# Kernel tuning notes

Hardware: AMD Instinct MI355X
Metric: run time of the kernel (lower is better)

The kernel has to match this reference:

```python
import jax, jax.numpy as jnp
import numpy as np

WS = 7  # window size of the inner WindowAttention
EPS = 1e-5


def pc_roll(xb, shifts, axis):
    """Per-channel circular roll of [B,C,H,W] along `axis` (2 or 3).
    torch.roll semantics: out[i] = in[(i - shift) % n]."""
    n = xb.shape[axis]
    idx = (jnp.arange(n)[None, :] - shifts[:, None]) % n  # [C, n]
    if axis == 2:
        idxb = jnp.broadcast_to(idx[None, :, :, None], xb.shape)
    else:
        idxb = jnp.broadcast_to(idx[None, :, None, :], xb.shape)
    return jnp.take_along_axis(xb, idxb, axis=axis)


def layernorm(x, w, b):
    m = x.mean(-1, keepdims=True)
    v = x.var(-1, keepdims=True)
    return (x - m) * jax.lax.rsqrt(v + EPS) * w + b


def batchnorm2d(x, g, b):
    # training-mode BN: batch statistics over (B,H,W) per channel
    m = x.mean(axis=(0, 2, 3), keepdims=True)
    v = x.var(axis=(0, 2, 3), keepdims=True)
    return (x - m) * jax.lax.rsqrt(v + EPS) * g[None, :, None, None] + b[None, :, None, None]


def conv1x1(x, w, b):
    # x: [B,C,H,W], w: [Cout,Cin]
    return jnp.einsum('bchw,oc->bohw', x, w) + b[None, :, None, None]


def window_attention(q, k, v):
    # single-head Swin-style window attention, 7x7 windows, no rel-pos bias
    B, C, H, W = q.shape
    nh, nw = H // WS, W // WS

    def part(t):  # [B,C,H,W] -> [B*nh*nw, WS*WS, C]
        t = t.reshape(B, C, nh, WS, nw, WS)
        return t.transpose(0, 2, 4, 3, 5, 1).reshape(B * nh * nw, WS * WS, C)

    qw, kw, vw = part(q), part(k), part(v)
    scale = C ** -0.5
    attn = jax.nn.softmax(jnp.einsum('wnc,wmc->wnm', qw, kw) * scale, axis=-1)
    out = jnp.einsum('wnm,wmc->wnc', attn, vw)
    out = out.reshape(B, nh, nw, WS, WS, C).transpose(0, 5, 1, 3, 2, 4).reshape(B, C, H, W)
    return out


def setup_inputs() -> dict:
    B, H, W, C = 32, 56, 56, 128
    N = H * W
    key = jax.random.key(0)
    ks = jax.random.split(key, 16)
    f32 = jnp.float32

    def lin_w(k, din, dout):
        return 0.02 * jax.random.normal(k, (din, dout), dtype=f32)

    conv_std = float(np.sqrt(2.0 / C))
    inp = {
        'x': jax.random.normal(ks[0], (B, N, C), dtype=f32),
        'fc1_w': lin_w(ks[1], C, C), 'fc1_b': jnp.zeros((C,), f32),
        'fc2_w': lin_w(ks[2], C, C), 'fc2_b': jnp.zeros((C,), f32),
        'fc3_w': lin_w(ks[3], C, C), 'fc3_b': jnp.zeros((C,), f32),
        'fc4_w': lin_w(ks[4], C, C), 'fc4_b': jnp.zeros((C,), f32),
        'fc5_w': lin_w(ks[5], 2 * C, C), 'fc5_b': jnp.zeros((C,), f32),
        'fc6_w': lin_w(ks[6], 2 * C, C), 'fc6_b': jnp.zeros((C,), f32),
        'ln_w': jnp.ones((2 * C,), f32), 'ln_b': jnp.zeros((2 * C,), f32),
        'q_w': conv_std * jax.random.normal(ks[7], (C, C), dtype=f32), 'q_b': jnp.zeros((C,), f32),
        'k_w': conv_std * jax.random.normal(ks[8], (C, C), dtype=f32), 'k_b': jnp.zeros((C,), f32),
        'v_w': conv_std * jax.random.normal(ks[9], (C, C), dtype=f32), 'v_b': jnp.zeros((C,), f32),
        'bn1_g': jnp.ones((C,), f32), 'bn1_b': jnp.zeros((C,), f32),
        'bn2_g': jnp.ones((C,), f32), 'bn2_b': jnp.zeros((C,), f32),
        'H': H, 'W': W,
    }
    return inp


def reference(x, fc1_w, fc1_b, fc2_w, fc2_b, fc3_w, fc3_b, fc4_w, fc4_b,
              fc5_w, fc5_b, fc6_w, fc6_b, ln_w, ln_b,
              q_w, q_b, k_w, k_b, v_w, v_b, bn1_g, bn1_b, bn2_g, bn2_b, H, W):
    B, N, C = x.shape
    shifts = jnp.arange(C)
    gelu = lambda t: jax.nn.gelu(t, approximate=False)

    def to_bchw(t):
        return t.transpose(0, 2, 1).reshape(B, C, H, W)

    def to_bnc(t):
        return t.reshape(B, C, N).transpose(0, 2, 1)

    # branch 1: roll +c along H -> fc1 -> GELU -> roll +c along W -> fc2
    h = to_bnc(pc_roll(to_bchw(x), shifts, axis=2))
    h = gelu(h @ fc1_w + fc1_b)
    h = to_bnc(pc_roll(to_bchw(h), shifts, axis=3))
    x_1 = h @ fc2_w + fc2_b

    # branch 2: roll -c along W -> fc3 -> GELU -> roll +c along H -> fc4
    h = to_bnc(pc_roll(to_bchw(x), -shifts, axis=3))
    h = gelu(h @ fc3_w + fc3_b)
    h = to_bnc(pc_roll(to_bchw(h), shifts, axis=2))
    x_2 = h @ fc4_w + fc4_b

    x_1 = x_1 + x
    x_2 = x_2 + x
    x1 = jnp.concatenate([x_1, x_2], axis=2)          # [B,N,2C]
    x1 = layernorm(x1, ln_w, ln_b)
    x1 = x1 @ fc5_w + fc5_b
    x1 = x1 + x

    # local-attention branch (DWConv module actually runs WindowAtten + BN + ReLU)
    xb = to_bchw(x)
    att = window_attention(conv1x1(xb, q_w, q_b), conv1x1(xb, k_w, k_b), conv1x1(xb, v_w, v_b))
    x2 = jax.nn.relu(batchnorm2d(att, bn1_g, bn1_b))  # DWConv forward
    x2 = jax.nn.relu(x2)                              # act2 (idempotent, kept for fidelity)
    x2 = batchnorm2d(x2, bn2_g, bn2_b)                # norm2
    x2 = x2.reshape(B, C, N).transpose(0, 2, 1)       # [B,N,C]

    x3 = jnp.concatenate([x1, x2], axis=2)            # [B,N,2C]
    return x3 @ fc6_w + fc6_b
```

## Files before the change

### kernel.cpp

```cpp
#include <hip/hip_runtime.h>
#include <hip/hip_bf16.h>
#include <cstdint>
#include <cstddef>

typedef __bf16 bf16_t;
typedef __bf16 bf16x8 __attribute__((ext_vector_type(8)));
typedef float f32x4 __attribute__((ext_vector_type(4)));

#define B_SZ 32
#define H_SZ 56
#define W_SZ 56
#define N_TOK 3136
#define CH 128
#define M_TOT 100352

#define WOFF_FC1 0
#define WOFF_FC2 16384
#define WOFF_FC3 32768
#define WOFF_FC4 49152
#define WOFF_FC5 65536
#define WOFF_FC6 98304
#define WOFF_QW  131072
#define WOFF_KW  147456
#define WOFF_VW  163840
#define WTOT     180224

enum { A_FLAT = 0, A_WROLL, A_LN, A_BN };
enum { E_BIAS = 0, E_GELU, E_RES };

__device__ __forceinline__ float bf2f(bf16_t v) { return (float)v; }
__device__ __forceinline__ unsigned short bfbits(float v) {
    bf16_t b = (bf16_t)v; unsigned short u; __builtin_memcpy(&u, &b, 2); return u;
}

__global__ __launch_bounds__(256)
void wcvt_k(const float* __restrict__ f1, const float* __restrict__ f2,
            const float* __restrict__ f3, const float* __restrict__ f4,
            const float* __restrict__ f5, const float* __restrict__ f6,
            const float* __restrict__ qw, const float* __restrict__ kw,
            const float* __restrict__ vw, bf16_t* __restrict__ wb)
{
    const int blk = blockIdx.x;
    const int tid = threadIdx.x;
    if (blk < 32) {
        __shared__ bf16_t T[64][72];
        const float* src; bf16_t* dst; int K, t;
        if (blk < 4)       { src = f1; dst = wb + WOFF_FC1; K = 128; t = blk; }
        else if (blk < 8)  { src = f2; dst = wb + WOFF_FC2; K = 128; t = blk - 4; }
        else if (blk < 12) { src = f3; dst = wb + WOFF_FC3; K = 128; t = blk - 8; }
        else if (blk < 16) { src = f4; dst = wb + WOFF_FC4; K = 128; t = blk - 12; }
        else if (blk < 24) { src = f5; dst = wb + WOFF_FC5; K = 256; t = blk - 16; }
        else               { src = f6; dst = wb + WOFF_FC6; K = 256; t = blk - 24; }
        const int ti = t >> 1;
        const int tj = t & 1;
        for (int it = tid; it < 64 * 16; it += 256) {
            const int r = it >> 4, c4 = it & 15;
            float4 u = *(const float4*)(src + (size_t)(ti * 64 + r) * 128 + tj * 64 + c4 * 4);
            T[c4 * 4 + 0][r] = (bf16_t)u.x;
            T[c4 * 4 + 1][r] = (bf16_t)u.y;
            T[c4 * 4 + 2][r] = (bf16_t)u.z;
            T[c4 * 4 + 3][r] = (bf16_t)u.w;
        }
        __syncthreads();
        for (int it = tid; it < 64 * 8; it += 256) {
            const int n = it >> 3, ck = it & 7;
            *(uint4*)(dst + (size_t)(tj * 64 + n) * K + ti * 64 + ck * 8) =
                *(const uint4*)(&T[n][ck * 8]);
        }
    } else {
        const float* src; bf16_t* dst;
        int t = blk - 32;
        if (t < 4)      { src = qw; dst = wb + WOFF_QW; }
        else if (t < 8) { src = kw; dst = wb + WOFF_KW; t -= 4; }
        else            { src = vw; dst = wb + WOFF_VW; t -= 8; }
        const int base = t * 4096 + tid * 16;
        float4 u0 = *(const float4*)(src + base);
        float4 u1 = *(const float4*)(src + base + 4);
        float4 u2 = *(const float4*)(src + base + 8);
        float4 u3 = *(const float4*)(src + base + 12);
        bf16_t o[16] = {(bf16_t)u0.x, (bf16_t)u0.y, (bf16_t)u0.z, (bf16_t)u0.w,
                        (bf16_t)u1.x, (bf16_t)u1.y, (bf16_t)u1.z, (bf16_t)u1.w,
                        (bf16_t)u2.x, (bf16_t)u2.y, (bf16_t)u2.z, (bf16_t)u2.w,
                        (bf16_t)u3.x, (bf16_t)u3.y, (bf16_t)u3.z, (bf16_t)u3.w};
        *(uint4*)(dst + base) = *(const uint4*)o;
        *(uint4*)(dst + base + 8) = *(const uint4*)(o + 8);
    }
}

__global__ __launch_bounds__(256)
void transpose_k(const float* __restrict__ x, bf16_t* __restrict__ xT)
{
    __shared__ bf16_t T[128][70];
    const int tid = threadIdx.x;
    const int mbase = blockIdx.x * 64;
    const int bimg = mbase / N_TOK;
    const int n0 = mbase - bimg * N_TOK;
    for (int idx = tid; idx < 64 * 32; idx += 256) {
        const int tok = idx >> 5, cg = idx & 31;
        float4 u = *(const float4*)(x + (size_t)(mbase + tok) * CH + cg * 4);
        T[cg * 4 + 0][tok] = (bf16_t)u.x;
        T[cg * 4 + 1][tok] = (bf16_t)u.y;
        T[cg * 4 + 2][tok] = (bf16_t)u.z;
        T[cg * 4 + 3][tok] = (bf16_t)u.w;
    }
    __syncthreads();
    const uint* T32 = (const uint*)&T[0][0];
    for (int idx = tid; idx < 128 * 8; idx += 256) {
        const int c = idx >> 3, chunk = idx & 7;
        uint4 o;
        o.x = T32[c * 35 + chunk * 4 + 0];
        o.y = T32[c * 35 + chunk * 4 + 1];
        o.z = T32[c * 35 + chunk * 4 + 2];
        o.w = T32[c * 35 + chunk * 4 + 3];
        *(uint4*)(xT + ((size_t)(bimg * 128 + c)) * N_TOK + n0 + chunk * 8) = o;
    }
}

template<int AMODE, int KHALVES, int EPI, int WDIR, int OTRANS, int OF32>
__global__ __launch_bounds__(256)
void gemm_k(const bf16_t* __restrict__ A0, const bf16_t* __restrict__ A1,
            const bf16_t* __restrict__ Wt, const float* __restrict__ bias,
            const float* __restrict__ resid,
            const float* __restrict__ rowst,
            const float* __restrict__ lnw, const float* __restrict__ lnb,
            const float* __restrict__ bnp,
            void* __restrict__ outv)
{
    __shared__ __align__(16) char smem[17920];
    bf16_t* As = (bf16_t*)smem;
    const int tid = threadIdx.x;
    const int mbase = blockIdx.x * 64;
    const int bimg = mbase / N_TOK;
    const int n0 = mbase - bimg * N_TOK;
    const int lane = tid & 63;
    const int wv = tid >> 6;
    const int qd = lane >> 4;
    const int mr = lane & 15;
    const int KS = 128 * KHALVES;

    f32x4 acc[4][2];
#pragma unroll
    for (int i = 0; i < 4; ++i)
#pragma unroll
        for (int j = 0; j < 2; ++j) { f32x4 z = {0.f,0.f,0.f,0.f}; acc[i][j] = z; }

    for (int kh = 0; kh < KHALVES; ++kh) {
        if (kh) __syncthreads();
        if (AMODE == A_FLAT || AMODE == A_WROLL) {
            for (int idx = tid; idx < 128 * 8; idx += 256) {
                const int c = idx >> 3, chunk = idx & 7;
                const int cm = (c >= 112) ? c - 112 : (c >= 56 ? c - 56 : c);
                const bf16_t* crow = A0 + ((size_t)(bimg * 128 + c)) * N_TOK;
                if (AMODE == A_FLAT) {
                    int t = n0 + chunk * 8 + N_TOK - 56 * cm;
                    if (t >= N_TOK) t -= N_TOK;
                    uint4 u = *(const uint4*)(crow + t);
                    const bf16_t* up = (const bf16_t*)&u;
#pragma unroll
                    for (int j = 0; j < 8; ++j) As[(chunk * 8 + j) * 136 + c] = up[j];
                } else {
                    const int nl = n0 + chunk * 8;
                    const int h = nl / 56;
                    const int w0 = nl - h * 56;
                    int ws = (WDIR > 0) ? (w0 + cm) : (w0 + 56 - cm);
                    if (ws >= 56) ws -= 56;
                    const bf16_t* hrow = crow + h * 56;
                    if (ws <= 48) {
                        uint4 u = *(const uint4*)(hrow + ws);
                        const bf16_t* up = (const bf16_t*)&u;
#pragma unroll
                        for (int j = 0; j < 8; ++j) As[(chunk * 8 + j) * 136 + c] = up[j];
                    } else {
#pragma unroll
                        for (int j = 0; j < 8; ++j) {
                            int wj = ws + j; if (wj >= 56) wj -= 56;
                            As[(chunk * 8 + j) * 136 + c] = hrow[wj];
                        }
                    }
                }
            }
        } else if (AMODE == A_LN) {
            for (int idx = tid; idx < 64 * 16; idx += 256) {
                const int row = idx >> 4, ck = idx & 15;
                const int rowg = mbase + row;
                const bf16_t* src = kh ? A1 : A0;
                uint4 u = *(const uint4*)(src + (size_t)rowg * CH + ck * 8);
                const bf16_t* up = (const bf16_t*)&u;
                const float mean = rowst[2 * rowg];
                const float rstd = rowst[2 * rowg + 1];
                const int cabs = kh * 128 + ck * 8;
                bf16_t t[8];
#pragma unroll
                for (int j = 0; j < 8; ++j) {
                    float v = (bf2f(up[j]) - mean) * rstd;
                    v = v * lnw[cabs + j] + lnb[cabs + j];
                    t[j] = (bf16_t)v;
                }
                *(uint4*)(&As[row * 136 + ck * 8]) = *(const uint4*)t;
            }
        } else {
            for (int idx = tid; idx < 64 * 16; idx += 256) {
                const int row = idx >> 4, ck = idx & 15;
                const int rowg = mbase + row;
                if (kh == 0) {
                    uint4 u = *(const uint4*)(A0 + (size_t)rowg * CH + ck * 8);
                    *(uint4*)(&As[row * 136 + ck * 8]) = u;
                } else {
                    uint4 u = *(const uint4*)(A1 + (size_t)rowg * CH + ck * 8);
                    const bf16_t* up = (const bf16_t*)&u;
                    bf16_t t[8];
#pragma unroll
                    for (int j = 0; j < 8; ++j) {
                        const int c = ck * 8 + j;
                        float z = fmaxf(0.f, bf2f(up[j]) * bnp[c] + bnp[128 + c]);
                        t[j] = (bf16_t)(z * bnp[256 + c] + bnp[384 + c]);
                    }
                    *(uint4*)(&As[row * 136 + ck * 8]) = *(const uint4*)t;
                }
            }
        }
        __syncthreads();
        const bf16_t* wbase = Wt + (size_t)(wv * 32 + mr) * KS + kh * 128 + qd * 8;
#pragma unroll
        for (int kt = 0; kt < 4; ++kt) {
            bf16x8 af[4], bfr[2];
#pragma unroll
            for (int mt = 0; mt < 4; ++mt)
                af[mt] = *(const bf16x8*)(&As[(mt * 16 + mr) * 136 + kt * 32 + qd * 8]);
#pragma unroll
            for (int nt = 0; nt < 2; ++nt)
                bfr[nt] = *(const bf16x8*)(wbase + (size_t)(nt * 16) * KS + kt * 32);
#pragma unroll
            for (int mt = 0; mt < 4; ++mt)
#pragma unroll
                for (int nt = 0; nt < 2; ++nt)
                    acc[mt][nt] = __builtin_amdgcn_mfma_f32_16x16x32_bf16(
                        af[mt], bfr[nt], acc[mt][nt], 0, 0, 0);
        }
    }
    if (OTRANS) {
        __syncthreads();
        uint* T32 = (uint*)smem;
#pragma unroll
        for (int mt = 0; mt < 4; ++mt)
#pragma unroll
            for (int nt = 0; nt < 2; ++nt) {
                const int col = wv * 32 + nt * 16 + mr;
                const float bb = bias[col];
#pragma unroll
                for (int rp = 0; rp < 2; ++rp) {
                    float v0 = acc[mt][nt][2 * rp] + bb;
                    float v1 = acc[mt][nt][2 * rp + 1] + bb;
                    if (EPI == E_GELU) {
                        v0 = 0.5f * v0 * (1.f + erff(v0 * 0.70710678118654752f));
                        v1 = 0.5f * v1 * (1.f + erff(v1 * 0.70710678118654752f));
                    }
                    T32[col * 35 + mt * 8 + qd * 2 + rp] =
                        (uint)bfbits(v0) | ((uint)bfbits(v1) << 16);
                }
            }
        __syncthreads();
        const int c = tid >> 1, half = tid & 1;
        uint r[16];
#pragma unroll
        for (int j = 0; j < 16; ++j) r[j] = T32[c * 35 + half * 16 + j];
        bf16_t* op = (bf16_t*)outv + ((size_t)(bimg * 128 + c)) * N_TOK + n0 + half * 32;
        uint4 o0 = {r[0], r[1], r[2], r[3]};
        uint4 o1 = {r[4], r[5], r[6], r[7]};
        uint4 o2 = {r[8], r[9], r[10], r[11]};
        uint4 o3 = {r[12], r[13], r[14], r[15]};
        ((uint4*)op)[0] = o0; ((uint4*)op)[1] = o1;
        ((uint4*)op)[2] = o2; ((uint4*)op)[3] = o3;
    } else {
#pragma unroll
        for (int mt = 0; mt < 4; ++mt)
#pragma unroll
            for (int nt = 0; nt < 2; ++nt) {
                const int col = wv * 32 + nt * 16 + mr;
                const float bb = bias[col];
#pragma unroll
                for (int r = 0; r < 4; ++r) {
                    const int rowg = mbase + mt * 16 + qd * 4 + r;
                    float v = acc[mt][nt][r] + bb;
                    if (EPI == E_GELU) v = 0.5f * v * (1.f + erff(v * 0.70710678118654752f));
                    if (EPI == E_RES)  v += resid[(size_t)rowg * CH + col];
                    if (OF32) ((float*)outv)[(size_t)rowg * CH + col] = v;
                    else ((bf16_t*)outv)[(size_t)rowg * CH + col] = (bf16_t)v;
                }
            }
    }
}

__global__ __launch_bounds__(256)
void qkv_k(const float* __restrict__ x, const bf16_t* __restrict__ wb,
           const float* __restrict__ qb, const float* __restrict__ kb,
           const float* __restrict__ vb,
           bf16_t* __restrict__ qo, bf16_t* __restrict__ ko, bf16_t* __restrict__ vo)
{
    __shared__ __align__(16) bf16_t As[64 * 136];
    const int tid = threadIdx.x;
    const int mbase = blockIdx.x * 64;
    const int lane = tid & 63;
    const int wv = tid >> 6;
    const int qd = lane >> 4;
    const int mr = lane & 15;

    for (int idx = tid; idx < 64 * 16; idx += 256) {
        const int row = idx >> 4, ck = idx & 15;
        const float* p = x + (size_t)(mbase + row) * CH + ck * 8;
        float4 u0 = *(const float4*)p;
        float4 u1 = *(const float4*)(p + 4);
        bf16_t t[8] = {(bf16_t)u0.x, (bf16_t)u0.y, (bf16_t)u0.z, (bf16_t)u0.w,
                       (bf16_t)u1.x, (bf16_t)u1.y, (bf16_t)u1.z, (bf16_t)u1.w};
        *(uint4*)(&As[row * 136 + ck * 8]) = *(const uint4*)t;
    }
    __syncthreads();
    bf16x8 af[4][4];
#pragma unroll
    for (int kt = 0; kt < 4; ++kt)
#pragma unroll
        for (int mt = 0; mt < 4; ++mt)
            af[kt][mt] = *(const bf16x8*)(&As[(mt * 16 + mr) * 136 + kt * 32 + qd * 8]);

    const int woffs[3] = {WOFF_QW, WOFF_KW, WOFF_VW};
    const float* bs3[3] = {qb, kb, vb};
    bf16_t* os3[3] = {qo, ko, vo};
#pragma unroll
    for (int s = 0; s < 3; ++s) {
        const bf16_t* wbase = wb + woffs[s] + (size_t)(wv * 32 + mr) * 128 + qd * 8;
        f32x4 acc[4][2];
#pragma unroll
        for (int i = 0; i < 4; ++i)
#pragma unroll
            for (int j = 0; j < 2; ++j) { f32x4 z = {0.f,0.f,0.f,0.f}; acc[i][j] = z; }
#pragma unroll
        for (int kt = 0; kt < 4; ++kt) {
            bf16x8 bfr[2];
#pragma unroll
            for (int nt = 0; nt < 2; ++nt)
                bfr[nt] = *(const bf16x8*)(wbase + (nt * 16) * 128 + kt * 32);
#pragma unroll
            for (int mt = 0; mt < 4; ++mt)
#pragma unroll
                for (int nt = 0; nt < 2; ++nt)
                    acc[mt][nt] = __builtin_amdgcn_mfma_f32_16x16x32_bf16(
                        af[kt][mt], bfr[nt], acc[mt][nt], 0, 0, 0);
        }
        bf16_t* out = os3[s];
#pragma unroll
        for (int mt = 0; mt < 4; ++mt)
#pragma unroll
            for (int nt = 0; nt < 2; ++nt) {
                const int col = wv * 32 + nt * 16 + mr;
                const float bb = bs3[s][col];
#pragma unroll
                for (int r = 0; r < 4; ++r) {
                    const int rowg = mbase + mt * 16 + qd * 4 + r;
                    out[(size_t)rowg * CH + col] = (bf16_t)(acc[mt][nt][r] + bb);
                }
            }
    }
}

__global__ __launch_bounds__(256)
void rowstats_k(const bf16_t* __restrict__ x1p, const bf16_t* __restrict__ x2p,
                float* __restrict__ rs)
{
    const int row = blockIdx.x * 4 + (threadIdx.x >> 6);
    const int lane = threadIdx.x & 63;
    const bf16_t* p1 = x1p + (size_t)row * CH + lane * 2;
    const bf16_t* p2 = x2p + (size_t)row * CH + lane * 2;
    float a0 = bf2f(p1[0]), a1 = bf2f(p1[1]);
    float b0 = bf2f(p2[0]), b1 = bf2f(p2[1]);
    float s = a0 + a1 + b0 + b1;
    float sq = a0 * a0 + a1 * a1 + b0 * b0 + b1 * b1;
#pragma unroll
    for (int off = 32; off > 0; off >>= 1) {
        s += __shfl_down(s, off);
        sq += __shfl_down(sq, off);
    }
    if (lane == 0) {
        float mean = s * (1.f / 256.f);
        float var = sq * (1.f / 256.f) - mean * mean;
        rs[2 * row] = mean;
        rs[2 * row + 1] = rsqrtf(var + 1e-5f);
    }
}

__global__ __launch_bounds__(256, 4)
void attn_k(const bf16_t* __restrict__ qg, const bf16_t* __restrict__ kg,
            const bf16_t* __restrict__ vg, bf16_t* __restrict__ og,
            float* __restrict__ partial)
{
    __shared__ __align__(16) bf16_t R0[64 * 136];
    __shared__ __align__(16) bf16_t R1[64 * 136];
    __shared__ float bnacc[256];
    const int tid = threadIdx.x;
    const int blk = blockIdx.x;
    const int b = blk >> 6;
    const int wy = (blk >> 3) & 7;
    const int wx = blk & 7;
    const int lane = tid & 63;
    const int wv = tid >> 6;
    const int qd = lane >> 4;
    const int mr = lane & 15;

    bnacc[tid] = 0.f;
    uint4 vreg[4];
    const int vc = tid & 127, vhalf = tid >> 7;
#pragma unroll
    for (int jc = 0; jc < 4; ++jc) {
        bf16_t t[8];
#pragma unroll
        for (int jj = 0; jj < 8; ++jj) {
            const int j = (vhalf * 4 + jc) * 8 + jj;
            bf16_t v = (bf16_t)0.f;
            if (j < 49) {
                const int n = (wy * 7 + j / 7) * 56 + wx * 7 + (j % 7);
                v = vg[((size_t)b * N_TOK + n) * CH + vc];
            }
            t[jj] = v;
        }
        vreg[jc] = *(const uint4*)t;
    }
    for (int idx = tid; idx < 64 * 16; idx += 256) {
        const int i = idx >> 4, ck = idx & 15;
        uint4 uq = {0, 0, 0, 0}, uk = {0, 0, 0, 0};
        if (i < 49) {
            const int n = (wy * 7 + i / 7) * 56 + wx * 7 + (i % 7);
            const size_t off = ((size_t)b * N_TOK + n) * CH + ck * 8;
            uq = *(const uint4*)(qg + off);
            uk = *(const uint4*)(kg + off);
        }
        *(uint4*)(&R0[i * 136 + ck * 8]) = uq;
        *(uint4*)(&R1[i * 136 + ck * 8]) = uk;
    }
    __syncthreads();
    bf16x8 aq[4];
#pragma unroll
    for (int kt = 0; kt < 4; ++kt)
        aq[kt] = *(const bf16x8*)(&R0[(wv * 16 + mr) * 136 + kt * 32 + qd * 8]);
    f32x4 sacc[4];
#pragma unroll
    for (int nt = 0; nt < 4; ++nt) {
        f32x4 a = {0.f, 0.f, 0.f, 0.f};
#pragma unroll
        for (int kt = 0; kt < 4; ++kt) {
            bf16x8 bk = *(const bf16x8*)(&R1[(nt * 16 + mr) * 136 + kt * 32 + qd * 8]);
            a = __builtin_amdgcn_mfma_f32_16x16x32_bf16(aq[kt], bk, a, 0, 0, 0);
        }
        sacc[nt] = a;
    }
    float* Ss = (float*)R0;
#pragma unroll
    for (int nt = 0; nt < 4; ++nt) {
        const int j = nt * 16 + mr;
#pragma unroll
        for (int r = 0; r < 4; ++r) {
            const int q = wv * 16 + qd * 4 + r;
            Ss[q * 68 + j] = (j < 49) ? sacc[nt][r] * 0.088388347648318447f : -1e30f;
        }
    }
    __syncthreads();
    {
        const int srow = tid >> 2, sq4 = tid & 3;
        const float* Sr = Ss + srow * 68 + sq4 * 16;
        float sv[16];
        *(float4*)(sv + 0)  = *(const float4*)(Sr + 0);
        *(float4*)(sv + 4)  = *(const float4*)(Sr + 4);
        *(float4*)(sv + 8)  = *(const float4*)(Sr + 8);
        *(float4*)(sv + 12) = *(const float4*)(Sr + 12);
        float mx = sv[0];
#pragma unroll
        for (int i = 1; i < 16; ++i) mx = fmaxf(mx, sv[i]);
        mx = fmaxf(mx, __shfl_xor(mx, 1));
        mx = fmaxf(mx, __shfl_xor(mx, 2));
        float sum = 0.f;
#pragma unroll
        for (int i = 0; i < 16; ++i) { sv[i] = __expf(sv[i] - mx); sum += sv[i]; }
        sum += __shfl_xor(sum, 1);
        sum += __shfl_xor(sum, 2);
        const float inv = 1.f / sum;
        __syncthreads();
        uint* P32 = (uint*)R1;
#pragma unroll
        for (int i = 0; i < 8; ++i) {
            const uint lo = bfbits(sv[2 * i] * inv);
            const uint hi = bfbits(sv[2 * i + 1] * inv);
            P32[srow * 36 + sq4 * 8 + i] = lo | (hi << 16);
        }
        bf16_t* Vt = R0;
#pragma unroll
        for (int jc = 0; jc < 4; ++jc)
            *(uint4*)(&Vt[vc * 68 + (vhalf * 4 + jc) * 8]) = vreg[jc];
    }
    __syncthreads();
    const bf16_t* Ps = R1;
    const bf16_t* Vt = R0;
    bf16x8 ap[2];
    ap[0] = *(const bf16x8*)(&Ps[(wv * 16 + mr) * 72 + qd * 8]);
    ap[1] = *(const bf16x8*)(&Ps[(wv * 16 + mr) * 72 + 32 + qd * 8]);
    f32x4 oacc[8];
#pragma unroll
    for (int nt = 0; nt < 8; ++nt) {
        f32x4 a = {0.f, 0.f, 0.f, 0.f};
#pragma unroll
        for (int kt = 0; kt < 2; ++kt) {
            bf16x8 bv = *(const bf16x8*)(&Vt[(nt * 16 + mr) * 68 + kt * 32 + qd * 8]);
            a = __builtin_amdgcn_mfma_f32_16x16x32_bf16(ap[kt], bv, a, 0, 0, 0);
        }
        oacc[nt] = a;
    }
#pragma unroll
    for (int nt = 0; nt < 8; ++nt) {
        const int c = nt * 16 + mr;
        float s = 0.f, sq = 0.f;
#pragma unroll
        for (int r = 0; r < 4; ++r) {
            const int q = wv * 16 + qd * 4 + r;
            if (q < 49) {
                const float v = oacc[nt][r];
                const int n = (wy * 7 + q / 7) * 56 + wx * 7 + (q % 7);
                og[((size_t)b * N_TOK + n) * CH + c] = (bf16_t)v;
                s += v; sq += v * v;
            }
        }
        atomicAdd(&bnacc[c], s);
        atomicAdd(&bnacc[128 + c], sq);
    }
    __syncthreads();
    partial[(size_t)blk * 256 + tid] = bnacc[tid];
}

__global__ __launch_bounds__(256)
void bnreduce_k(const float* __restrict__ partial, float* __restrict__ accum)
{
    const int t = threadIdx.x;
    const int r0 = blockIdx.x * 16;
    float s = 0.f;
#pragma unroll
    for (int r = 0; r < 16; ++r) s += partial[(size_t)(r0 + r) * 256 + t];
    atomicAdd(&accum[t], s);
}

__global__ __launch_bounds__(256)
void bnstats2_k(const bf16_t* __restrict__ att, const float* __restrict__ g1,
                const float* __restrict__ b1, float* __restrict__ accum)
{
    __shared__ float ls[256], lq[256];
    const int c = threadIdx.x & 127;
    const int half = threadIdx.x >> 7;
    const float m = accum[c] * (1.f / (float)M_TOT);
    const float var = accum[128 + c] * (1.f / (float)M_TOT) - m * m;
    const float rstd = rsqrtf(var + 1e-5f);
    const float scl = g1[c] * rstd;
    const float sh = b1[c] - m * scl;
    const size_t rowbase = (size_t)blockIdx.x * 196;
    float s = 0.f, sq = 0.f;
    for (int r = half; r < 196; r += 2) {
        float z = fmaxf(0.f, bf2f(att[(rowbase + r) * CH + c]) * scl + sh);
        s += z; sq += z * z;
    }
    ls[threadIdx.x] = s; lq[threadIdx.x] = sq;
    __syncthreads();
    if (threadIdx.x < 128) {
        atomicAdd(&accum[256 + c], ls[threadIdx.x] + ls[threadIdx.x + 128]);
        atomicAdd(&accum[384 + c], lq[threadIdx.x] + lq[threadIdx.x + 128]);
    }
}

__global__ void bnparams_k(const float* __restrict__ accum,
                           const float* __restrict__ g1, const float* __restrict__ b1,
                           const float* __restrict__ g2, const float* __restrict__ b2,
                           float* __restrict__ bnp)
{
    const int c = threadIdx.x;
    const float inv = 1.f / (float)M_TOT;
    float m1 = accum[c] * inv;
    float v1 = accum[128 + c] * inv - m1 * m1;
    float rs1 = rsqrtf(v1 + 1e-5f);
    float s1 = g1[c] * rs1;
    float sh1 = b1[c] - m1 * s1;
    float m2 = accum[256 + c] * inv;
    float v2 = accum[384 + c] * inv - m2 * m2;
    float rs2 = rsqrtf(v2 + 1e-5f);
    float s2 = g2[c] * rs2;
    float sh2 = b2[c] - m2 * s2;
    bnp[c] = s1; bnp[128 + c] = sh1; bnp[256 + c] = s2; bnp[384 + c] = sh2;
}

__global__ void zero_k(float* __restrict__ p) { p[threadIdx.x] = 0.f; }

extern "C" void kernel_launch(void* const* d_in, const int* in_sizes, int n_in,
                              void* d_out, int out_size, void* d_ws, size_t ws_size,
                              hipStream_t stream)
{
    (void)in_sizes; (void)n_in; (void)out_size; (void)ws_size;
    const float* x     = (const float*)d_in[0];
    const float* fc1_w = (const float*)d_in[1];
    const float* fc1_b = (const float*)d_in[2];
    const float* fc2_w = (const float*)d_in[3];
    const float* fc2_b = (const float*)d_in[4];
    const float* fc3_w = (const float*)d_in[5];
    const float* fc3_b = (const float*)d_in[6];
    const float* fc4_w = (const float*)d_in[7];
    const float* fc4_b = (const float*)d_in[8];
    const float* fc5_w = (const float*)d_in[9];
    const float* fc5_b = (const float*)d_in[10];
    const float* fc6_w = (const float*)d_in[11];
    const float* fc6_b = (const float*)d_in[12];
    const float* ln_w  = (const float*)d_in[13];
    const float* ln_b  = (const float*)d_in[14];
    const float* q_w   = (const float*)d_in[15];
    const float* q_b   = (const float*)d_in[16];
    const float* k_w   = (const float*)d_in[17];
    const float* k_b   = (const float*)d_in[18];
    const float* v_w   = (const float*)d_in[19];
    const float* v_b   = (const float*)d_in[20];
    const float* bn1_g = (const float*)d_in[21];
    const float* bn1_b = (const float*)d_in[22];
    const float* bn2_g = (const float*)d_in[23];
    const float* bn2_b = (const float*)d_in[24];

    char* ws = (char*)d_ws;
    const size_t SZB = (size_t)M_TOT * CH * sizeof(bf16_t);
    bf16_t* bufA = (bf16_t*)(ws);
    bf16_t* bufB = (bf16_t*)(ws + SZB);
    bf16_t* bufC = (bf16_t*)(ws + 2 * SZB);
    bf16_t* bufD = (bf16_t*)(ws + 3 * SZB);
    float*  rs   = (float*)(ws + 4 * SZB);
    float*  accum = (float*)(ws + 4 * SZB + (size_t)M_TOT * 2 * sizeof(float));
    float*  bnp  = accum + 512;
    float*  partial = bnp + 512;
    bf16_t* wbuf = (bf16_t*)(partial + 2048 * 256);

    const dim3 blk(256);
    const int GG = M_TOT / 64;

    zero_k<<<1, 512, 0, stream>>>(accum);
    wcvt_k<<<44, blk, 0, stream>>>(fc1_w, fc2_w, fc3_w, fc4_w, fc5_w, fc6_w,
                                   q_w, k_w, v_w, wbuf);
    transpose_k<<<GG, blk, 0, stream>>>(x, bufA);
    gemm_k<A_FLAT, 1, E_GELU, 0, 1, 0><<<GG, blk, 0, stream>>>(
        bufA, nullptr, wbuf + WOFF_FC1, fc1_b, nullptr, nullptr, nullptr, nullptr, nullptr, bufB);
    gemm_k<A_WROLL, 1, E_RES, -1, 0, 0><<<GG, blk, 0, stream>>>(
        bufB, nullptr, wbuf + WOFF_FC2, fc2_b, x, nullptr, nullptr, nullptr, nullptr, bufC);
    gemm_k<A_WROLL, 1, E_GELU, 1, 1, 0><<<GG, blk, 0, stream>>>(
        bufA, nullptr, wbuf + WOFF_FC3, fc3_b, nullptr, nullptr, nullptr, nullptr, nullptr, bufB);
    gemm_k<A_FLAT, 1, E_RES, 0, 0, 0><<<GG, blk, 0, stream>>>(
        bufB, nullptr, wbuf + WOFF_FC4, fc4_b, x, nullptr, nullptr, nullptr, nullptr, bufD);
    rowstats_k<<<M_TOT / 4, blk, 0, stream>>>(bufC, bufD, rs);
    gemm_k<A_LN, 2, E_RES, 0, 0, 0><<<GG, blk, 0, stream>>>(
        bufC, bufD, wbuf + WOFF_FC5, fc5_b, x, rs, ln_w, ln_b, nullptr, bufB);
    qkv_k<<<GG, blk, 0, stream>>>(x, wbuf, q_b, k_b, v_b, bufA, bufC, bufD);
    attn_k<<<B_SZ * 64, blk, 0, stream>>>(bufA, bufC, bufD, bufA, partial);
    bnreduce_k<<<128, blk, 0, stream>>>(partial, accum);
    bnstats2_k<<<512, blk, 0, stream>>>(bufA, bn1_g, bn1_b, accum);
    bnparams_k<<<1, 128, 0, stream>>>(accum, bn1_g, bn1_b, bn2_g, bn2_b, bnp);
    gemm_k<A_BN, 2, E_BIAS, 0, 0, 1><<<GG, blk, 0, stream>>>(
        bufB, bufA, wbuf + WOFF_FC6, fc6_b, nullptr, nullptr, nullptr, nullptr, bnp, d_out);
}
```

Before: 486.3 us.

## Restructure window attention kernel memory traffic and shrink shared memory

The window attention kernel now loads Q and K straight from global memory into MFMA operand registers, skipping the LDS staging. V is loaded with coalesced 16-byte reads and transposed through LDS rather than gathered with scattered 2-byte global loads. The output goes through an LDS tile and is written as coalesced 16-byte stores. The BN partial sums are reduced across lanes with shuffles before the shared atomics. Shared memory drops to about 35 KB through buffer aliasing, which may raise occupancy, at the cost of redundant global reads of K across waves and extra barriers.

```diff
diff --git a/kernel.cpp b/kernel.cpp
--- a/kernel.cpp
+++ b/kernel.cpp
@@ -392,9 +392,14 @@
             const bf16_t* __restrict__ vg, bf16_t* __restrict__ og,
             float* __restrict__ partial)
 {
-    __shared__ __align__(16) bf16_t R0[64 * 136];
-    __shared__ __align__(16) bf16_t R1[64 * 136];
-    __shared__ float bnacc[256];
+    __shared__ __align__(16) char smem[35840];
+    bf16_t* Vr = (bf16_t*)smem;
+    float*  Ss = (float*)smem;
+    bf16_t* Ps = (bf16_t*)smem;
+    bf16_t* Vt = (bf16_t*)(smem + 17408);
+    bf16_t* Os = (bf16_t*)smem;
+    float* bnacc = (float*)(smem + 34816);
+
     const int tid = threadIdx.x;
     const int blk = blockIdx.x;
     const int b = blk >> 6;
@@ -406,52 +411,59 @@
     const int mr = lane & 15;
 
     bnacc[tid] = 0.f;
-    uint4 vreg[4];
-    const int vc = tid & 127, vhalf = tid >> 7;
-#pragma unroll
-    for (int jc = 0; jc < 4; ++jc) {
-        bf16_t t[8];
-#pragma unroll
-        for (int jj = 0; jj < 8; ++jj) {
-            const int j = (vhalf * 4 + jc) * 8 + jj;
-            bf16_t v = (bf16_t)0.f;
-            if (j < 49) {
-                const int n = (wy * 7 + j / 7) * 56 + wx * 7 + (j % 7);
-                v = vg[((size_t)b * N_TOK + n) * CH + vc];
-            }
-            t[jj] = v;
-        }
-        vreg[jc] = *(const uint4*)t;
-    }
+
     for (int idx = tid; idx < 64 * 16; idx += 256) {
         const int i = idx >> 4, ck = idx & 15;
-        uint4 uq = {0, 0, 0, 0}, uk = {0, 0, 0, 0};
+        uint4 uv = {0, 0, 0, 0};
         if (i < 49) {
             const int n = (wy * 7 + i / 7) * 56 + wx * 7 + (i % 7);
-            const size_t off = ((size_t)b * N_TOK + n) * CH + ck * 8;
-            uq = *(const uint4*)(qg + off);
-            uk = *(const uint4*)(kg + off);
-        }
-        *(uint4*)(&R0[i * 136 + ck * 8]) = uq;
-        *(uint4*)(&R1[i * 136 + ck * 8]) = uk;
-    }
-    __syncthreads();
+            uv = *(const uint4*)(vg + ((size_t)b * N_TOK + n) * CH + ck * 8);
+        }
+        *(uint4*)(&Vr[i * 136 + ck * 8]) = uv;
+    }
+    __syncthreads();
+
+    const int vc = tid & 127, vhalf = tid >> 7;
+    {
+        uint4 vreg[4];
+#pragma unroll
+        for (int jc = 0; jc < 4; ++jc) {
+            bf16_t t[8];
+#pragma unroll
+            for (int jj = 0; jj < 8; ++jj)
+                t[jj] = Vr[(vhalf * 32 + jc * 8 + jj) * 136 + vc];
+            vreg[jc] = *(const uint4*)t;
+        }
+#pragma unroll
+        for (int jc = 0; jc < 4; ++jc)
+            *(uint4*)(&Vt[vc * 68 + (vhalf * 4 + jc) * 8]) = vreg[jc];
+    }
+    __syncthreads();
+
+    const int qrow = wv * 16 + mr;
+    const int qc = qrow < 49 ? qrow : 48;
+    const bf16_t* qptr = qg + ((size_t)b * N_TOK +
+                               (wy * 7 + qc / 7) * 56 + wx * 7 + (qc % 7)) * CH + qd * 8;
     bf16x8 aq[4];
 #pragma unroll
     for (int kt = 0; kt < 4; ++kt)
-        aq[kt] = *(const bf16x8*)(&R0[(wv * 16 + mr) * 136 + kt * 32 + qd * 8]);
+        aq[kt] = *(const bf16x8*)(qptr + kt * 32);
+
     f32x4 sacc[4];
 #pragma unroll
     for (int nt = 0; nt < 4; ++nt) {
+        const int krow = nt * 16 + mr;
+        const int kc = krow < 49 ? krow : 48;
+        const bf16_t* kptr = kg + ((size_t)b * N_TOK +
+                                   (wy * 7 + kc / 7) * 56 + wx * 7 + (kc % 7)) * CH + qd * 8;
         f32x4 a = {0.f, 0.f, 0.f, 0.f};
 #pragma unroll
         for (int kt = 0; kt < 4; ++kt) {
-            bf16x8 bk = *(const bf16x8*)(&R1[(nt * 16 + mr) * 136 + kt * 32 + qd * 8]);
+            bf16x8 bk = *(const bf16x8*)(kptr + kt * 32);
             a = __builtin_amdgcn_mfma_f32_16x16x32_bf16(aq[kt], bk, a, 0, 0, 0);
         }
         sacc[nt] = a;
     }
-    float* Ss = (float*)R0;
 #pragma unroll
     for (int nt = 0; nt < 4; ++nt) {
         const int j = nt * 16 + mr;
@@ -462,6 +474,7 @@
         }
     }
     __syncthreads();
+
     {
         const int srow = tid >> 2, sq4 = tid & 3;
         const float* Sr = Ss + srow * 68 + sq4 * 16;
@@ -482,21 +495,16 @@
         sum += __shfl_xor(sum, 2);
         const float inv = 1.f / sum;
         __syncthreads();
-        uint* P32 = (uint*)R1;
+        uint* P32 = (uint*)smem;
 #pragma unroll
         for (int i = 0; i < 8; ++i) {
             const uint lo = bfbits(sv[2 * i] * inv);
             const uint hi = bfbits(sv[2 * i + 1] * inv);
             P32[srow * 36 + sq4 * 8 + i] = lo | (hi << 16);
         }
-        bf16_t* Vt = R0;
-#pragma unroll
-        for (int jc = 0; jc < 4; ++jc)
-            *(uint4*)(&Vt[vc * 68 + (vhalf * 4 + jc) * 8]) = vreg[jc];
-    }
-    __syncthreads();
-    const bf16_t* Ps = R1;
-    const bf16_t* Vt = R0;
+    }
+    __syncthreads();
+
     bf16x8 ap[2];
     ap[0] = *(const bf16x8*)(&Ps[(wv * 16 + mr) * 72 + qd * 8]);
     ap[1] = *(const bf16x8*)(&Ps[(wv * 16 + mr) * 72 + 32 + qd * 8]);
@@ -511,6 +519,7 @@
         }
         oacc[nt] = a;
     }
+
 #pragma unroll
     for (int nt = 0; nt < 8; ++nt) {
         const int c = nt * 16 + mr;
@@ -518,17 +527,31 @@
 #pragma unroll
         for (int r = 0; r < 4; ++r) {
             const int q = wv * 16 + qd * 4 + r;
-            if (q < 49) {
-                const float v = oacc[nt][r];
-                const int n = (wy * 7 + q / 7) * 56 + wx * 7 + (q % 7);
-                og[((size_t)b * N_TOK + n) * CH + c] = (bf16_t)v;
-                s += v; sq += v * v;
-            }
-        }
-        atomicAdd(&bnacc[c], s);
-        atomicAdd(&bnacc[128 + c], sq);
-    }
-    __syncthreads();
+            if (q < 49) { const float v = oacc[nt][r]; s += v; sq += v * v; }
+        }
+        s += __shfl_xor(s, 16); sq += __shfl_xor(sq, 16);
+        s += __shfl_xor(s, 32); sq += __shfl_xor(sq, 32);
+        if (qd == 0) { atomicAdd(&bnacc[c], s); atomicAdd(&bnacc[128 + c], sq); }
+    }
+    __syncthreads();
+
+#pragma unroll
+    for (int nt = 0; nt < 8; ++nt) {
+        const int c = nt * 16 + mr;
+#pragma unroll
+        for (int r = 0; r < 4; ++r) {
+            const int q = wv * 16 + qd * 4 + r;
+            Os[q * 140 + c] = (bf16_t)oacc[nt][r];
+        }
+    }
+    __syncthreads();
+
+    for (int idx = tid; idx < 49 * 16; idx += 256) {
+        const int row = idx >> 4, u = idx & 15;
+        const int n = (wy * 7 + row / 7) * 56 + wx * 7 + (row % 7);
+        *(uint4*)(og + ((size_t)b * N_TOK + n) * CH + u * 8) =
+            *(const uint4*)(&Os[row * 140 + u * 8]);
+    }
     partial[(size_t)blk * 256 + tid] = bnacc[tid];
 }
 
```

Result: faster. 468.6 us (-3.6%).
